# Performance work log

Measured on AMD Instinct MI355X. Metric: run time of the kernel, lower is better.

## Reference

```python
import jax, jax.numpy as jnp
import numpy as np
import math

C = 256

def conv_bn_lrelu(x, w, scale, bias, dilation):
    # Conv2d(k=3, stride=1, padding=dilation, dilation=dilation, bias=False) + eval BN (folded) + LeakyReLU(0.1)
    d = dilation
    y = jax.lax.conv_general_dilated(
        x, w, window_strides=(1, 1), padding=[(d, d), (d, d)],
        rhs_dilation=(d, d), dimension_numbers=('NCHW', 'OIHW', 'NCHW'))
    y = y * scale[None, :, None, None] + bias[None, :, None, None]
    return jnp.where(y > 0, y, 0.1 * y)

def unfold3x3(x):
    # [b,c,h,w] -> [b,c,9,h,w]: 3x3 neighborhoods (zero pad 1), row-major window order like F.unfold
    b, c, h, w = x.shape
    xp = jnp.pad(x, ((0, 0), (0, 0), (1, 1), (1, 1)))
    return jnp.stack([xp[:, :, i:i + h, j:j + w] for i in range(3) for j in range(3)], axis=2)

def self_attn(Q, K, V):
    b, c, h, w = Q.shape
    Ku = unfold3x3(K)                     # [b,c,9,h,w]
    Vu = unfold3x3(V)                     # [b,c,9,h,w]
    dot = Q[:, :, None] * Ku * (1.0 / math.sqrt(c))
    dot = jax.nn.softmax(dot, axis=2)     # softmax over 9 neighbors, per channel
    return jnp.sum(dot * Vu, axis=2)      # [b,c,h,w]

def setup_inputs() -> dict:
    key = jax.random.key(0)
    ks = jax.random.split(key, 20)
    fan = C * 9
    wstd = math.sqrt(2.0 / fan)
    def w(k):
        return jax.random.normal(k, (C, C, 3, 3), dtype=jnp.float32) * wstd
    def s(k):
        return jax.random.uniform(k, (C,), dtype=jnp.float32, minval=0.5, maxval=1.5)
    def b(k):
        return jax.random.normal(k, (C,), dtype=jnp.float32) * 0.1
    inp = {'x': jax.random.normal(ks[0], (4, C, 64, 64), dtype=jnp.float32)}
    names = ['q1', 'k1', 'v1', 'q2', 'k2', 'v2']
    for i, n in enumerate(names):
        inp[n[0] + 'w' + n[1]] = w(ks[1 + 3 * i])
        inp[n[0] + 's' + n[1]] = s(ks[2 + 3 * i])
        inp[n[0] + 'b' + n[1]] = b(ks[3 + 3 * i])
    return inp

def reference(x, qw1, qs1, qb1, kw1, ks1, kb1, vw1, vs1, vb1,
              qw2, qs2, qb2, kw2, ks2, kb2, vw2, vs2, vb2):
    Q1 = conv_bn_lrelu(x, qw1, qs1, qb1, dilation=1)
    K1 = conv_bn_lrelu(x, kw1, ks1, kb1, dilation=1)
    V1 = conv_bn_lrelu(x, vw1, vs1, vb1, dilation=1)
    attn1 = self_attn(Q1, K1, V1)
    Q2 = conv_bn_lrelu(attn1, qw2, qs2, qb2, dilation=2)
    K2 = conv_bn_lrelu(attn1, kw2, ks2, kb2, dilation=2)
    V2 = conv_bn_lrelu(attn1, vw2, vs2, vb2, dilation=2)
    return self_attn(Q2, K2, V2)
```

## Files before the change

### kernel.cpp

```cpp
#include <hip/hip_runtime.h>
#include <stdint.h>

typedef __attribute__((ext_vector_type(8))) short short8;
typedef __attribute__((ext_vector_type(4))) float f32x4;
typedef __attribute__((ext_vector_type(4))) unsigned short u16x4;
typedef __attribute__((ext_vector_type(8))) unsigned short u16x8;

#define DEV static __device__ __forceinline__

DEV unsigned short f2bf(float f) {
  unsigned u = __float_as_uint(f);
  u += 0x7FFFu + ((u >> 16) & 1u);
  return (unsigned short)(u >> 16);
}
DEV float bf2f(unsigned short s) { return __uint_as_float(((unsigned)s) << 16); }

DEV void gload16(const void* g, void* l) {
  __attribute__((address_space(1))) unsigned* gp =
      reinterpret_cast<__attribute__((address_space(1))) unsigned*>(
          reinterpret_cast<uintptr_t>(g));
  __attribute__((address_space(3))) unsigned* lp =
      reinterpret_cast<__attribute__((address_space(3))) unsigned*>(
          reinterpret_cast<uintptr_t>(l));
  __builtin_amdgcn_global_load_lds(gp, lp, 16, 0, 0);
}

__global__ __launch_bounds__(256) void prep_w6(
    const float* __restrict__ w0, const float* __restrict__ s0,
    const float* __restrict__ w1, const float* __restrict__ s1,
    const float* __restrict__ w2, const float* __restrict__ s2,
    const float* __restrict__ w3, const float* __restrict__ s3,
    const float* __restrict__ w4, const float* __restrict__ s4,
    const float* __restrict__ w5, const float* __restrict__ s5,
    unsigned short* __restrict__ W2base) {
  const int set = blockIdx.y;
  const float* wl[6] = {w0, w1, w2, w3, w4, w5};
  const float* sl[6] = {s0, s1, s2, s3, s4, s5};
  const float* w = wl[set];
  const float* sc = sl[set];
  unsigned short* W2 = W2base + (size_t)set * 256 * 2304;
  const int e = blockIdx.x * 256 + threadIdx.x;
  const int cout = e / 2304;
  const int r = e - cout * 2304;
  const int tap = r >> 8;
  const int cin = r & 255;
  W2[e] = f2bf(w[(size_t)(cout * 256 + cin) * 9 + tap] * sc[cout]);
}

__global__ __launch_bounds__(256) void zero_borders(
    unsigned short* __restrict__ XP, unsigned short* __restrict__ QP,
    unsigned short* __restrict__ KP, unsigned short* __restrict__ VP,
    unsigned short* __restrict__ AP) {
  const int buf = blockIdx.y >> 2, b = blockIdx.y & 3;
  const int P = (buf == 4) ? 68 : 66;
  const int pad = (buf == 4) ? 2 : 1;
  const int nb = P * P - 64 * 64;
  const int i = blockIdx.x * 256 + threadIdx.x;
  const int pxi = i >> 5, ch = (i & 31) * 8;
  if (pxi >= nb) return;
  const int topbot = 2 * pad * P;
  int h, w;
  if (pxi < topbot) {
    const int r = pxi / P, c = pxi - r * P;
    h = (r < pad) ? r : P - 2 * pad + r;
    w = c;
  } else {
    const int j = pxi - topbot;
    const int r = j / (2 * pad), c = j - r * 2 * pad;
    h = pad + r;
    w = (c < pad) ? c : P - 2 * pad + c;
  }
  unsigned short* base = buf == 0 ? XP : buf == 1 ? QP : buf == 2 ? KP
                         : buf == 3 ? VP : AP;
  const u16x8 z = {0, 0, 0, 0, 0, 0, 0, 0};
  *(u16x8*)&base[((size_t)(b * P + h) * P + w) * 256 + ch] = z;
}

__global__ __launch_bounds__(256) void pad_cast(const float* __restrict__ x,
                                                unsigned short* __restrict__ Xp) {
  const int gid = blockIdx.x * 256 + threadIdx.x;
  const int cch = gid & 31;
  const int pix = gid >> 5;
  const int b = pix >> 12, h = (pix >> 6) & 63, w = pix & 63;
  const int c0 = cch * 8;
  const float* src = x + ((size_t)(b * 256 + c0) * 64 + h) * 64 + w;
  u16x8 o;
#pragma unroll
  for (int i = 0; i < 8; ++i) o[i] = f2bf(src[(size_t)i * 4096]);
  *(u16x8*)&Xp[((size_t)(b * 66 + h + 1) * 66 + (w + 1)) * 256 + c0] = o;
}

template <int D>
__global__ __launch_bounds__(256, 2) void conv_qkv(
    const unsigned short* __restrict__ Xp, const unsigned short* __restrict__ Wq,
    const unsigned short* __restrict__ Wk, const unsigned short* __restrict__ Wv,
    const float* __restrict__ bq, const float* __restrict__ bk,
    const float* __restrict__ bv, unsigned short* __restrict__ Qo,
    unsigned short* __restrict__ Ko, unsigned short* __restrict__ Vo) {
  constexpr int P = 64 + 2 * D;
  constexpr int HALF = 128 * 64 + 3 * 64 * 64;
  __shared__ __align__(16) unsigned short lds[2 * HALF];

  const int tid = threadIdx.x;
  const int lane = tid & 63;
  const int wid = tid >> 6;
  const int wm = wid >> 1;
  const int wn = wid & 1;
  const int m0 = blockIdx.x * 64;
  const int rg = blockIdx.y;
  const int b = rg >> 5;
  const int h0 = (rg & 31) * 2;

  f32x4 acc[3][2][4];
#pragma unroll
  for (int c = 0; c < 3; ++c)
#pragma unroll
    for (int m = 0; m < 2; ++m)
#pragma unroll
      for (int n = 0; n < 4; ++n) acc[c][m][n] = (f32x4){0.f, 0.f, 0.f, 0.f};

  const int w0i = tid >> 3;
  const int j3 = (tid & 7) ^ (w0i & 7);
  const unsigned short* wptr[3] = {Wq, Wk, Wv};
  size_t bRow[2];
#pragma unroll
  for (int r = 0; r < 2; ++r)
    bRow[r] = ((size_t)(b * P + h0 + r) * P + w0i) * 256 + j3 * 8;
  const size_t aBase = (size_t)(m0 + w0i) * 2304 + j3 * 8;

  auto STAGE = [&](int s, int hf) {
    const int t = s >> 2, kb = s & 3;
    const int ty = t / 3, tx = t - ty * 3;
    const size_t tapOff = ((size_t)(ty * D) * P + tx * D) * 256 + kb * 64;
    const int kOff = t * 256 + kb * 64;
    unsigned short* base = &lds[hf * HALF];
#pragma unroll
    for (int k = 0; k < 4; ++k)
      gload16(Xp + bRow[k >> 1] + (size_t)(32 * (k & 1)) * 256 + tapOff,
              &base[(k * 256 + tid) * 8]);
#pragma unroll
    for (int k = 0; k < 6; ++k)
      gload16(wptr[k >> 1] + aBase + (size_t)(k & 1) * 32 * 2304 + kOff,
              &base[8192 + (k * 256 + tid) * 8]);
  };

  auto COMPUTE = [&](int hf) {
    const unsigned short* base = &lds[hf * HALF];
#pragma unroll
    for (int kk = 0; kk < 2; ++kk) {
      const int jc = kk * 4 + (lane >> 4);
      short8 bfr[4], afr[3][2];
#pragma unroll
      for (int n = 0; n < 4; ++n) {
        const int row = wn * 64 + n * 16 + (lane & 15);
        bfr[n] = *(const short8*)&base[row * 64 + ((jc ^ (row & 7)) << 3)];
      }
#pragma unroll
      for (int c = 0; c < 3; ++c)
#pragma unroll
        for (int m = 0; m < 2; ++m) {
          const int row = wm * 32 + m * 16 + (lane & 15);
          afr[c][m] = *(const short8*)&base[8192 + c * 4096 + row * 64 +
                                            ((jc ^ (row & 7)) << 3)];
        }
#pragma unroll
      for (int c = 0; c < 3; ++c)
#pragma unroll
        for (int m = 0; m < 2; ++m)
#pragma unroll
          for (int n = 0; n < 4; ++n)
            acc[c][m][n] = __builtin_amdgcn_mfma_f32_16x16x32_bf16(
                afr[c][m], bfr[n], acc[c][m][n], 0, 0, 0);
    }
  };

  STAGE(0, 0);
#pragma unroll 1
  for (int s = 0; s < 35; ++s) {
    const int p = s & 1;
    STAGE(s + 1, p ^ 1);
    asm volatile("s_waitcnt vmcnt(10)" ::: "memory");
    __builtin_amdgcn_s_barrier();
    COMPUTE(p);
    __builtin_amdgcn_s_barrier();
  }
  asm volatile("s_waitcnt vmcnt(0)" ::: "memory");
  __builtin_amdgcn_s_barrier();
  COMPUTE(1);

  const float* bias[3] = {bq, bk, bv};
  unsigned short* outp[3] = {Qo, Ko, Vo};
  const int r4 = (lane >> 4) << 2;
#pragma unroll
  for (int c = 0; c < 3; ++c) {
#pragma unroll
    for (int m = 0; m < 2; ++m) {
      const int cout = m0 + wm * 32 + m * 16 + r4;
      const f32x4 bb = *(const f32x4*)&bias[c][cout];
#pragma unroll
      for (int n = 0; n < 4; ++n) {
        const int px = wn * 64 + n * 16 + (lane & 15);
        const int ww = px & 63;
        const int hh = h0 + (px >> 6);
        const size_t off =
            ((size_t)(b * 66 + hh + 1) * 66 + (ww + 1)) * 256 + cout;
        u16x4 pk;
#pragma unroll
        for (int r = 0; r < 4; ++r) {
          float f = acc[c][m][n][r] + bb[r];
          f = f > 0.f ? f : 0.1f * f;
          pk[r] = f2bf(f);
        }
        *(u16x4*)&outp[c][off] = pk;
      }
    }
  }
}

template <int MODE>
__global__ __launch_bounds__(256) void attn3x3(
    const unsigned short* __restrict__ Qp, const unsigned short* __restrict__ Kp,
    const unsigned short* __restrict__ Vp, unsigned short* __restrict__ outB,
    float* __restrict__ outF) {
  __shared__ float so[8][257];
  const int tid = threadIdx.x;
  const int gid = blockIdx.x * 256 + tid;
  const int cch = gid & 31;
  const int pix = gid >> 5;
  const int b = pix >> 12, h = (pix >> 6) & 63, w = pix & 63;
  const int c0 = cch * 8;

  const size_t cen = ((size_t)(b * 66 + h + 1) * 66 + (w + 1)) * 256 + c0;
  const size_t tl = ((size_t)(b * 66 + h) * 66 + w) * 256 + c0;

  float q[8];
  {
    u16x8 u = *(const u16x8*)&Qp[cen];
#pragma unroll
    for (int i = 0; i < 8; ++i) q[i] = bf2f(u[i]) * 0.0625f;
  }
  float s[9][8];
#pragma unroll
  for (int t = 0; t < 9; ++t) {
    u16x8 u = *(const u16x8*)&Kp[tl + (size_t)((t / 3) * 66 + (t % 3)) * 256];
#pragma unroll
    for (int i = 0; i < 8; ++i) s[t][i] = q[i] * bf2f(u[i]);
  }
  float mx[8];
#pragma unroll
  for (int i = 0; i < 8; ++i) {
    float m = s[0][i];
#pragma unroll
    for (int t = 1; t < 9; ++t) m = fmaxf(m, s[t][i]);
    mx[i] = m;
  }
  float num[8], den[8];
#pragma unroll
  for (int i = 0; i < 8; ++i) { num[i] = 0.f; den[i] = 0.f; }
#pragma unroll
  for (int t = 0; t < 9; ++t) {
    u16x8 u = *(const u16x8*)&Vp[tl + (size_t)((t / 3) * 66 + (t % 3)) * 256];
#pragma unroll
    for (int i = 0; i < 8; ++i) {
      const float e = __expf(s[t][i] - mx[i]);
      den[i] += e;
      num[i] += e * bf2f(u[i]);
    }
  }

  if (MODE == 0) {
    u16x8 o;
#pragma unroll
    for (int i = 0; i < 8; ++i) o[i] = f2bf(num[i] / den[i]);
    *(u16x8*)&outB[((size_t)(b * 68 + h + 2) * 68 + (w + 2)) * 256 + c0] = o;
  } else {
    const int ps = tid >> 5;
#pragma unroll
    for (int i = 0; i < 8; ++i) so[ps][c0 + i] = num[i] / den[i];
    __syncthreads();
    const int pix0 = blockIdx.x * 8;
    const int b2 = pix0 >> 12, h2 = (pix0 >> 6) & 63, w0 = pix0 & 63;
    const int c = tid;
    const size_t ob = (((size_t)b2 * 256 + c) * 64 + h2) * 64 + w0;
    f32x4 v0 = (f32x4){so[0][c], so[1][c], so[2][c], so[3][c]};
    f32x4 v1 = (f32x4){so[4][c], so[5][c], so[6][c], so[7][c]};
    *(f32x4*)&outF[ob] = v0;
    *(f32x4*)&outF[ob + 4] = v1;
  }
}

extern "C" void kernel_launch(void* const* d_in, const int* in_sizes, int n_in,
                              void* d_out, int out_size, void* d_ws,
                              size_t ws_size, hipStream_t stream) {
  (void)in_sizes; (void)n_in; (void)out_size; (void)ws_size;
  const float* x = (const float*)d_in[0];
  const float* wqs[6] = {(const float*)d_in[1],  (const float*)d_in[4],
                         (const float*)d_in[7],  (const float*)d_in[10],
                         (const float*)d_in[13], (const float*)d_in[16]};
  const float* scs[6] = {(const float*)d_in[2],  (const float*)d_in[5],
                         (const float*)d_in[8],  (const float*)d_in[11],
                         (const float*)d_in[14], (const float*)d_in[17]};
  const float* bq1 = (const float*)d_in[3];
  const float* bk1 = (const float*)d_in[6];
  const float* bv1 = (const float*)d_in[9];
  const float* bq2 = (const float*)d_in[12];
  const float* bk2 = (const float*)d_in[15];
  const float* bv2 = (const float*)d_in[18];

  char* ws = (char*)d_ws;
  const size_t SZ66 = (size_t)4 * 66 * 66 * 256 * 2;
  const size_t SZ68 = (size_t)4 * 68 * 68 * 256 * 2;
  unsigned short* XP = (unsigned short*)(ws);
  unsigned short* QP = (unsigned short*)(ws + SZ66);
  unsigned short* KP = (unsigned short*)(ws + 2 * SZ66);
  unsigned short* VP = (unsigned short*)(ws + 3 * SZ66);
  unsigned short* AP = (unsigned short*)(ws + 4 * SZ66);
  const size_t wbase = 4 * SZ66 + SZ68;
  unsigned short* W2base = (unsigned short*)(ws + wbase);
  const size_t WSET = (size_t)256 * 2304;

  zero_borders<<<dim3(66, 20), 256, 0, stream>>>(XP, QP, KP, VP, AP);
  prep_w6<<<dim3(2304, 6), 256, 0, stream>>>(
      wqs[0], scs[0], wqs[1], scs[1], wqs[2], scs[2], wqs[3], scs[3], wqs[4],
      scs[4], wqs[5], scs[5], W2base);
  pad_cast<<<2048, 256, 0, stream>>>(x, XP);

  conv_qkv<1><<<dim3(4, 128), 256, 0, stream>>>(
      XP, W2base, W2base + WSET, W2base + 2 * WSET, bq1, bk1, bv1, QP, KP, VP);
  attn3x3<0><<<2048, 256, 0, stream>>>(QP, KP, VP, AP, nullptr);
  conv_qkv<2><<<dim3(4, 128), 256, 0, stream>>>(
      AP, W2base + 3 * WSET, W2base + 4 * WSET, W2base + 5 * WSET, bq2, bk2,
      bv2, QP, KP, VP);
  attn3x3<1><<<2048, 256, 0, stream>>>(QP, KP, VP, nullptr, (float*)d_out);
}
```

Baseline: 186.9 us.

## Coalesce prep and pad kernels, remap blocks across XCDs, raise MFMA priority

The weight-prep kernel now has each thread read the 9 contiguous taps of one (cout, cin) pair and write them with coalesced strides. pad_cast stages a channel-by-width tile in LDS so that both the NCHW reads and the NHWC bf16 writes are coalesced. The conv and attention grids are flattened and remapped so that blocks landing on the same XCD work on neighbouring spatial rows, which should improve L2 reuse of shared input rows. s_setprio is raised around the MFMA block so a wave's matrix instructions get issue priority over other waves' loads. Together these target uncoalesced memory traffic in the prep kernels and cache locality in the main kernels, at the cost of more complex index arithmetic.

Result: faster. 163.7 us (-12.4%).

```diff
diff --git a/kernel.cpp b/kernel.cpp
--- a/kernel.cpp
+++ b/kernel.cpp
@@ -36,15 +36,17 @@
   const int set = blockIdx.y;
   const float* wl[6] = {w0, w1, w2, w3, w4, w5};
   const float* sl[6] = {s0, s1, s2, s3, s4, s5};
-  const float* w = wl[set];
-  const float* sc = sl[set];
-  unsigned short* W2 = W2base + (size_t)set * 256 * 2304;
-  const int e = blockIdx.x * 256 + threadIdx.x;
-  const int cout = e / 2304;
-  const int r = e - cout * 2304;
-  const int tap = r >> 8;
-  const int cin = r & 255;
-  W2[e] = f2bf(w[(size_t)(cout * 256 + cin) * 9 + tap] * sc[cout]);
+  const int cout = blockIdx.x;
+  const int t = threadIdx.x;
+  const float sc = sl[set][cout];
+  const float* src = wl[set] + ((size_t)cout * 256 + t) * 9;
+  float v[9];
+#pragma unroll
+  for (int k = 0; k < 9; ++k) v[k] = src[k] * sc;
+  unsigned short* dst =
+      W2base + (size_t)set * 256 * 2304 + (size_t)cout * 2304;
+#pragma unroll
+  for (int k = 0; k < 9; ++k) dst[k * 256 + t] = f2bf(v[k]);
 }
 
 __global__ __launch_bounds__(256) void zero_borders(
@@ -78,16 +80,29 @@
 
 __global__ __launch_bounds__(256) void pad_cast(const float* __restrict__ x,
                                                 unsigned short* __restrict__ Xp) {
-  const int gid = blockIdx.x * 256 + threadIdx.x;
-  const int cch = gid & 31;
-  const int pix = gid >> 5;
-  const int b = pix >> 12, h = (pix >> 6) & 63, w = pix & 63;
-  const int c0 = cch * 8;
-  const float* src = x + ((size_t)(b * 256 + c0) * 64 + h) * 64 + w;
-  u16x8 o;
-#pragma unroll
-  for (int i = 0; i < 8; ++i) o[i] = f2bf(src[(size_t)i * 4096]);
-  *(u16x8*)&Xp[((size_t)(b * 66 + h + 1) * 66 + (w + 1)) * 256 + c0] = o;
+  __shared__ float sm[64][65];
+  const int bid = blockIdx.x;
+  const int ct = bid & 3;
+  const int h = (bid >> 2) & 63;
+  const int b = bid >> 8;
+  const int t = threadIdx.x;
+  const int wl = t & 63, cr = t >> 6;
+#pragma unroll
+  for (int cc = 0; cc < 16; ++cc) {
+    const int c = cc * 4 + cr;
+    sm[c][wl] = x[((size_t)(b * 256 + ct * 64 + c) * 64 + h) * 64 + wl];
+  }
+  __syncthreads();
+  const int ww = t >> 2, c16 = (t & 3) * 16;
+  u16x8 o0, o1;
+#pragma unroll
+  for (int i = 0; i < 8; ++i) o0[i] = f2bf(sm[c16 + i][ww]);
+#pragma unroll
+  for (int i = 0; i < 8; ++i) o1[i] = f2bf(sm[c16 + 8 + i][ww]);
+  const size_t base =
+      ((size_t)(b * 66 + h + 1) * 66 + (ww + 1)) * 256 + ct * 64 + c16;
+  *(u16x8*)&Xp[base] = o0;
+  *(u16x8*)&Xp[base + 8] = o1;
 }
 
 template <int D>
@@ -106,8 +121,10 @@
   const int wid = tid >> 6;
   const int wm = wid >> 1;
   const int wn = wid & 1;
-  const int m0 = blockIdx.x * 64;
-  const int rg = blockIdx.y;
+  const int wgid = blockIdx.x;
+  const int xcd = wgid & 7;
+  const int m0 = (xcd & 3) * 64;
+  const int rg = (wgid >> 3) + 64 * (xcd >> 2);
   const int b = rg >> 5;
   const int h0 = (rg & 31) * 2;
 
@@ -163,6 +180,7 @@
           afr[c][m] = *(const short8*)&base[8192 + c * 4096 + row * 64 +
                                             ((jc ^ (row & 7)) << 3)];
         }
+      __builtin_amdgcn_s_setprio(1);
 #pragma unroll
       for (int c = 0; c < 3; ++c)
 #pragma unroll
@@ -171,6 +189,7 @@
           for (int n = 0; n < 4; ++n)
             acc[c][m][n] = __builtin_amdgcn_mfma_f32_16x16x32_bf16(
                 afr[c][m], bfr[n], acc[c][m][n], 0, 0, 0);
+      __builtin_amdgcn_s_setprio(0);
     }
   };
 
@@ -224,7 +243,8 @@
     float* __restrict__ outF) {
   __shared__ float so[8][257];
   const int tid = threadIdx.x;
-  const int gid = blockIdx.x * 256 + tid;
+  const int bid = ((blockIdx.x & 7) << 8) + (blockIdx.x >> 3);
+  const int gid = bid * 256 + tid;
   const int cch = gid & 31;
   const int pix = gid >> 5;
   const int b = pix >> 12, h = (pix >> 6) & 63, w = pix & 63;
@@ -278,7 +298,7 @@
 #pragma unroll
     for (int i = 0; i < 8; ++i) so[ps][c0 + i] = num[i] / den[i];
     __syncthreads();
-    const int pix0 = blockIdx.x * 8;
+    const int pix0 = bid * 8;
     const int b2 = pix0 >> 12, h2 = (pix0 >> 6) & 63, w0 = pix0 & 63;
     const int c = tid;
     const size_t ob = (((size_t)b2 * 256 + c) * 64 + h2) * 64 + w0;
@@ -320,15 +340,15 @@
   const size_t WSET = (size_t)256 * 2304;
 
   zero_borders<<<dim3(66, 20), 256, 0, stream>>>(XP, QP, KP, VP, AP);
-  prep_w6<<<dim3(2304, 6), 256, 0, stream>>>(
+  prep_w6<<<dim3(256, 6), 256, 0, stream>>>(
       wqs[0], scs[0], wqs[1], scs[1], wqs[2], scs[2], wqs[3], scs[3], wqs[4],
       scs[4], wqs[5], scs[5], W2base);
-  pad_cast<<<2048, 256, 0, stream>>>(x, XP);
-
-  conv_qkv<1><<<dim3(4, 128), 256, 0, stream>>>(
+  pad_cast<<<1024, 256, 0, stream>>>(x, XP);
+
+  conv_qkv<1><<<512, 256, 0, stream>>>(
       XP, W2base, W2base + WSET, W2base + 2 * WSET, bq1, bk1, bv1, QP, KP, VP);
   attn3x3<0><<<2048, 256, 0, stream>>>(QP, KP, VP, AP, nullptr);
-  conv_qkv<2><<<dim3(4, 128), 256, 0, stream>>>(
+  conv_qkv<2><<<512, 256, 0, stream>>>(
       AP, W2base + 3 * WSET, W2base + 4 * WSET, W2base + 5 * WSET, bq2, bk2,
       bv2, QP, KP, VP);
   attn3x3<1><<<2048, 256, 0, stream>>>(QP, KP, VP, nullptr, (float*)d_out);
```
